# Optimization experiments

Hardware: AMD Instinct MI355X
Metric: run time of the kernel (lower is better)

## Reference

```python
import jax, jax.numpy as jnp
import numpy as np

B, H, W = 8, 640, 640
NUM_INST = 16  # upper bound on instance ids; segment reduce handles absent ids


def _bce(p, t):
    # torch BCELoss clamps log terms at -100
    lp = jnp.clip(jnp.log(p), -100.0)
    l1p = jnp.clip(jnp.log1p(-p), -100.0)
    return -(t * lp + (1.0 - t) * l1p)


def setup_inputs() -> dict:
    key = jax.random.key(0)
    k1, k2, k3, k4 = jax.random.split(key, 4)
    preds = jax.random.uniform(k1, (B, 2, H, W), dtype=jnp.float32,
                               minval=1e-4, maxval=1.0 - 1e-4)
    conf = jax.random.bernoulli(k2, 0.3, (B, H, W)).astype(jnp.float32)
    overlap = jax.random.bernoulli(k3, 0.1, (B, H, W)).astype(jnp.float32)
    inst = jax.random.randint(k4, (B, H, W), 0, NUM_INST, dtype=jnp.int32)
    inds = jnp.arange(B, dtype=jnp.int64) if jax.config.jax_enable_x64 else jnp.arange(B, dtype=jnp.int32)
    return {"preds": preds, "conf": conf, "inst": inst,
            "overlap": overlap, "inds": inds}


def reference(preds, conf, inst, overlap, inds):
    p1 = preds[:, 0]
    p2 = preds[:, 1]
    and_preds = p1 * p2
    and_loss_map = _bce(and_preds, overlap)            # [B,H,W]
    or_loss = _bce(jnp.maximum(p1, p2), conf).mean()
    and_overlap = and_preds * overlap
    op1 = jnp.maximum(p1, and_overlap)
    op2 = jnpp = jnp.maximum(p2, and_overlap)

    b, h, w = p1.shape
    # per-(sample, instance-id) segment reduce replacing the python loops.
    # MSELoss(bop*mask, mask)/sum(mask) == segment-mean of (op-1)^2 over the mask.
    seg = (jnp.arange(b, dtype=jnp.int32)[:, None, None] * NUM_INST + inst).reshape(-1)
    e1 = ((op1 - 1.0) ** 2).reshape(-1)
    e2 = ((op2 - 1.0) ** 2).reshape(-1)
    nseg = b * NUM_INST
    cnt = jax.ops.segment_sum(jnp.ones_like(e1), seg, num_segments=nseg).reshape(b, NUM_INST)
    s1 = jax.ops.segment_sum(e1, seg, num_segments=nseg).reshape(b, NUM_INST)
    s2 = jax.ops.segment_sum(e2, seg, num_segments=nseg).reshape(b, NUM_INST)
    present = cnt > 0
    safe_cnt = jnp.where(present, cnt, 1.0)
    d1 = s1 / safe_cnt
    d2 = s2 / safe_cnt
    # min(d1,d2) - max(d1,d2) + 1 == 1 - |d1 - d2|, only for present keys
    per_key = jnp.where(present, 1.0 - jnp.abs(d1 - d2), 0.0)
    nkeys = present.sum(axis=1).astype(p1.dtype)       # torch.unique count per sample
    inst_loss = (per_key.sum(axis=1) / nkeys).mean()

    pos = (conf == 1).astype(p1.dtype)
    neg = (conf == 0).astype(p1.dtype)
    and_loss = (and_loss_map * pos).sum() / pos.sum() + (and_loss_map * neg).sum() / neg.sum()

    return 0.5 * and_loss + 0.25 * or_loss + 0.25 * inst_loss
```

## Files before the change

kernel.cpp:

```cpp
#include <hip/hip_runtime.h>
#include <hip/hip_bf16.h>

#define BB 8
#define HH 640
#define WW 640
#define HWN (HH * WW)
#define NUM_INST 16
#define NBLK 128
#define NBLK_TOT (NBLK * BB)
#define THREADS 256
#define NV 36


__device__ __forceinline__ void process_pixel(
    float p1, float p2, float c, float t, int k,
    float* s12, float* cnt,
    float& accPos, float& accAll, float& accOr, float& accCnt)
{
    float andp = p1 * p2;
    bool tpos = (t != 0.0f);
    bool cpos = (c != 0.0f);
    float argA = tpos ? andp : (1.0f - andp);
    float bce_and = -fmaxf(__logf(argA), -100.0f);
    accAll += bce_and;
    accPos += cpos ? bce_and : 0.0f;
    accCnt += c;
    float mx = fmaxf(p1, p2);
    float argO = cpos ? mx : (1.0f - mx);
    accOr -= fmaxf(__logf(argO), -100.0f);
    float ao = tpos ? andp : 0.0f;
    float d1 = fmaxf(p1, ao) - 1.0f;
    float d2 = fmaxf(p2, ao) - 1.0f;
    float e12 = (d1 - d2) * (d1 + d2);
    #pragma unroll
    for (int j = 0; j < NUM_INST; ++j) {
        bool m = (k == j);
        s12[j] += m ? e12  : 0.0f;
        cnt[j] += m ? 1.0f : 0.0f;
    }
}

__global__ __launch_bounds__(THREADS) void overlap_main_kernel(
    const float* __restrict__ preds, const float* __restrict__ conf,
    const int* __restrict__ inst, const float* __restrict__ overlap,
    float* __restrict__ ws)
{
    const int b   = blockIdx.y;
    const int tid = threadIdx.x;

    const float4* p1v = (const float4*)(preds + (size_t)b * 2 * HWN);
    const float4* p2v = (const float4*)(preds + (size_t)b * 2 * HWN + HWN);
    const float4* cv  = (const float4*)(conf    + (size_t)b * HWN);
    const float4* tv  = (const float4*)(overlap + (size_t)b * HWN);
    const int4*   kv  = (const int4*)(inst      + (size_t)b * HWN);

    float vals[NV];
    #pragma unroll
    for (int v = 0; v < NV; ++v) vals[v] = 0.0f;
    float* s12 = vals;
    float* cnt = vals + 16;
    float& accPos = vals[32];
    float& accAll = vals[33];
    float& accOr  = vals[34];
    float& accCnt = vals[35];

    const int nvec   = HWN / 4;
    const int stride = gridDim.x * blockDim.x;
    for (int i = blockIdx.x * blockDim.x + tid; i < nvec; i += stride) {
        float4 A = p1v[i];
        float4 B = p2v[i];
        float4 C = cv[i];
        float4 T = tv[i];
        int4   K = kv[i];
        process_pixel(A.x, B.x, C.x, T.x, K.x, s12, cnt, accPos, accAll, accOr, accCnt);
        process_pixel(A.y, B.y, C.y, T.y, K.y, s12, cnt, accPos, accAll, accOr, accCnt);
        process_pixel(A.z, B.z, C.z, T.z, K.z, s12, cnt, accPos, accAll, accOr, accCnt);
        process_pixel(A.w, B.w, C.w, T.w, K.w, s12, cnt, accPos, accAll, accOr, accCnt);
    }

    #pragma unroll
    for (int s = 32; s > 0; s >>= 1) {
        #pragma unroll
        for (int v = 0; v < NV; ++v) vals[v] += __shfl_xor(vals[v], s, 64);
    }

    __shared__ float wsum[4][NV];
    const int wave = tid >> 6;
    const int lane = tid & 63;
    if (lane == 0) {
        #pragma unroll
        for (int v = 0; v < NV; ++v) wsum[wave][v] = vals[v];
    }
    __syncthreads();
    if (tid < NV) {
        float s = wsum[0][tid] + wsum[1][tid] + wsum[2][tid] + wsum[3][tid];
        int g = blockIdx.y * NBLK + blockIdx.x;
        ws[tid * NBLK_TOT + g] = s;
    }
}

__global__ __launch_bounds__(320) void overlap_finalize_kernel(
    const float* __restrict__ ws, float* __restrict__ out)
{
    __shared__ float seg[BB][NV];
    __shared__ float perkey[BB][NUM_INST];
    __shared__ float pres[BB][NUM_INST];
    __shared__ float binst[BB];
    const int t = threadIdx.x;

    if (t < BB * NV) {
        int b = t / NV, v = t % NV;
        const float4* p = (const float4*)(ws + v * NBLK_TOT + b * NBLK);
        float4 s4 = {0.0f, 0.0f, 0.0f, 0.0f};
        #pragma unroll 8
        for (int i = 0; i < NBLK / 4; ++i) {
            float4 q = p[i];
            s4.x += q.x; s4.y += q.y; s4.z += q.z; s4.w += q.w;
        }
        seg[b][v] = (s4.x + s4.y) + (s4.z + s4.w);
    }
    __syncthreads();

    if (t < BB * NUM_INST) {
        int b = t >> 4, k = t & 15;
        float c = seg[b][16 + k];
        bool present = c > 0.0f;
        float sc = present ? c : 1.0f;
        perkey[b][k] = present ? (1.0f - fabsf(seg[b][k]) / sc) : 0.0f;
        pres[b][k]   = present ? 1.0f : 0.0f;
    }
    __syncthreads();

    if (t < BB) {
        float s = 0.0f, nk = 0.0f;
        for (int k = 0; k < NUM_INST; ++k) { s += perkey[t][k]; nk += pres[t][k]; }
        binst[t] = s / nk;
    }
    __syncthreads();

    if (t == 0) {
        float instLoss = 0.0f, posS = 0.0f, allS = 0.0f, orS = 0.0f, posC = 0.0f;
        for (int b = 0; b < BB; ++b) {
            instLoss += binst[b];
            posS += seg[b][32];
            allS += seg[b][33];
            orS  += seg[b][34];
            posC += seg[b][35];
        }
        instLoss *= (1.0f / (float)BB);
        const float N = (float)BB * (float)HWN;
        float negS = allS - posS;
        float andLoss = posS / posC + negS / (N - posC);
        float orLoss  = orS / N;
        out[0] = 0.5f * andLoss + 0.25f * orLoss + 0.25f * instLoss;
    }
}

extern "C" void kernel_launch(void* const* d_in, const int* in_sizes, int n_in,
                              void* d_out, int out_size, void* d_ws, size_t ws_size,
                              hipStream_t stream) {
    const float* preds   = (const float*)d_in[0];
    const float* conf    = (const float*)d_in[1];
    const int*   inst    = (const int*)d_in[2];
    const float* overlap = (const float*)d_in[3];
    float* ws  = (float*)d_ws;
    float* out = (float*)d_out;

    dim3 grid(NBLK, BB);
    overlap_main_kernel<<<grid, THREADS, 0, stream>>>(preds, conf, inst, overlap, ws);
    overlap_finalize_kernel<<<1, 320, 0, stream>>>(ws, out);
}
```

Baseline: 112.5 us.

## Use exact-fit grid with all loads hoisted and ballot-based instance counts

```diff
diff --git a/kernel.cpp b/kernel.cpp
--- a/kernel.cpp
+++ b/kernel.cpp
@@ -6,25 +6,26 @@
 #define WW 640
 #define HWN (HH * WW)
 #define NUM_INST 16
-#define NBLK 128
+#define NBLK 200
 #define NBLK_TOT (NBLK * BB)
 #define THREADS 256
 #define NV 36
+#define HALF_VEC (NBLK * THREADS)
 
 
 __device__ __forceinline__ void process_pixel(
     float p1, float p2, float c, float t, int k,
-    float* s12, float* cnt,
-    float& accPos, float& accAll, float& accOr, float& accCnt)
+    float* s12, unsigned* cnt_s,
+    float& accPos, float& accAll, float& accOr, unsigned& posCnt)
 {
     float andp = p1 * p2;
     bool tpos = (t != 0.0f);
     bool cpos = (c != 0.0f);
     float argA = tpos ? andp : (1.0f - andp);
-    float bce_and = -fmaxf(__logf(argA), -100.0f);
-    accAll += bce_and;
-    accPos += cpos ? bce_and : 0.0f;
-    accCnt += c;
+    float bce = -fmaxf(__logf(argA), -100.0f);
+    accAll += bce;
+    accPos += cpos ? bce : 0.0f;
+    posCnt += (unsigned)__popcll(__ballot(cpos));
     float mx = fmaxf(p1, p2);
     float argO = cpos ? mx : (1.0f - mx);
     accOr -= fmaxf(__logf(argO), -100.0f);
@@ -35,8 +36,8 @@
     #pragma unroll
     for (int j = 0; j < NUM_INST; ++j) {
         bool m = (k == j);
-        s12[j] += m ? e12  : 0.0f;
-        cnt[j] += m ? 1.0f : 0.0f;
+        s12[j] += m ? e12 : 0.0f;
+        cnt_s[j] += (unsigned)__popcll(__ballot(m));
     }
 }
 
@@ -47,6 +48,8 @@
 {
     const int b   = blockIdx.y;
     const int tid = threadIdx.x;
+    const int i0  = blockIdx.x * THREADS + tid;
+    const int i1  = i0 + HALF_VEC;
 
     const float4* p1v = (const float4*)(preds + (size_t)b * 2 * HWN);
     const float4* p2v = (const float4*)(preds + (size_t)b * 2 * HWN + HWN);
@@ -54,34 +57,36 @@
     const float4* tv  = (const float4*)(overlap + (size_t)b * HWN);
     const int4*   kv  = (const int4*)(inst      + (size_t)b * HWN);
 
-    float vals[NV];
+    float4 A0 = p1v[i0]; float4 A1 = p1v[i1];
+    float4 B0 = p2v[i0]; float4 B1 = p2v[i1];
+    float4 C0 = cv[i0];  float4 C1 = cv[i1];
+    float4 T0 = tv[i0];  float4 T1 = tv[i1];
+    int4   K0 = kv[i0];  int4   K1 = kv[i1];
+
+    float s12[NUM_INST];
+    unsigned cnt_s[NUM_INST];
     #pragma unroll
-    for (int v = 0; v < NV; ++v) vals[v] = 0.0f;
-    float* s12 = vals;
-    float* cnt = vals + 16;
-    float& accPos = vals[32];
-    float& accAll = vals[33];
-    float& accOr  = vals[34];
-    float& accCnt = vals[35];
+    for (int j = 0; j < NUM_INST; ++j) { s12[j] = 0.0f; cnt_s[j] = 0u; }
+    float accPos = 0.0f, accAll = 0.0f, accOr = 0.0f;
+    unsigned posCnt = 0u;
 
-    const int nvec   = HWN / 4;
-    const int stride = gridDim.x * blockDim.x;
-    for (int i = blockIdx.x * blockDim.x + tid; i < nvec; i += stride) {
-        float4 A = p1v[i];
-        float4 B = p2v[i];
-        float4 C = cv[i];
-        float4 T = tv[i];
-        int4   K = kv[i];
-        process_pixel(A.x, B.x, C.x, T.x, K.x, s12, cnt, accPos, accAll, accOr, accCnt);
-        process_pixel(A.y, B.y, C.y, T.y, K.y, s12, cnt, accPos, accAll, accOr, accCnt);
-        process_pixel(A.z, B.z, C.z, T.z, K.z, s12, cnt, accPos, accAll, accOr, accCnt);
-        process_pixel(A.w, B.w, C.w, T.w, K.w, s12, cnt, accPos, accAll, accOr, accCnt);
-    }
+    process_pixel(A0.x, B0.x, C0.x, T0.x, K0.x, s12, cnt_s, accPos, accAll, accOr, posCnt);
+    process_pixel(A0.y, B0.y, C0.y, T0.y, K0.y, s12, cnt_s, accPos, accAll, accOr, posCnt);
+    process_pixel(A0.z, B0.z, C0.z, T0.z, K0.z, s12, cnt_s, accPos, accAll, accOr, posCnt);
+    process_pixel(A0.w, B0.w, C0.w, T0.w, K0.w, s12, cnt_s, accPos, accAll, accOr, posCnt);
+    process_pixel(A1.x, B1.x, C1.x, T1.x, K1.x, s12, cnt_s, accPos, accAll, accOr, posCnt);
+    process_pixel(A1.y, B1.y, C1.y, T1.y, K1.y, s12, cnt_s, accPos, accAll, accOr, posCnt);
+    process_pixel(A1.z, B1.z, C1.z, T1.z, K1.z, s12, cnt_s, accPos, accAll, accOr, posCnt);
+    process_pixel(A1.w, B1.w, C1.w, T1.w, K1.w, s12, cnt_s, accPos, accAll, accOr, posCnt);
 
+    float fv[19];
+    #pragma unroll
+    for (int j = 0; j < NUM_INST; ++j) fv[j] = s12[j];
+    fv[16] = accPos; fv[17] = accAll; fv[18] = accOr;
     #pragma unroll
     for (int s = 32; s > 0; s >>= 1) {
         #pragma unroll
-        for (int v = 0; v < NV; ++v) vals[v] += __shfl_xor(vals[v], s, 64);
+        for (int v = 0; v < 19; ++v) fv[v] += __shfl_xor(fv[v], s, 64);
     }
 
     __shared__ float wsum[4][NV];
@@ -89,7 +94,14 @@
     const int lane = tid & 63;
     if (lane == 0) {
         #pragma unroll
-        for (int v = 0; v < NV; ++v) wsum[wave][v] = vals[v];
+        for (int j = 0; j < NUM_INST; ++j) {
+            wsum[wave][j]      = fv[j];
+            wsum[wave][16 + j] = (float)cnt_s[j];
+        }
+        wsum[wave][32] = fv[16];
+        wsum[wave][33] = fv[17];
+        wsum[wave][34] = fv[18];
+        wsum[wave][35] = (float)posCnt;
     }
     __syncthreads();
     if (tid < NV) {
@@ -99,7 +111,7 @@
     }
 }
 
-__global__ __launch_bounds__(320) void overlap_finalize_kernel(
+__global__ __launch_bounds__(576) void overlap_finalize_kernel(
     const float* __restrict__ ws, float* __restrict__ out)
 {
     __shared__ float seg[BB][NV];
@@ -108,16 +120,19 @@
     __shared__ float binst[BB];
     const int t = threadIdx.x;
 
-    if (t < BB * NV) {
-        int b = t / NV, v = t % NV;
-        const float4* p = (const float4*)(ws + v * NBLK_TOT + b * NBLK);
-        float4 s4 = {0.0f, 0.0f, 0.0f, 0.0f};
-        #pragma unroll 8
-        for (int i = 0; i < NBLK / 4; ++i) {
+    {
+        int row  = t >> 1;
+        int half = t & 1;
+        int b = row / NV, v = row - b * NV;
+        const float4* p = (const float4*)(ws + v * NBLK_TOT + b * NBLK) + half * 25;
+        float s = 0.0f;
+        #pragma unroll
+        for (int i = 0; i < 25; ++i) {
             float4 q = p[i];
-            s4.x += q.x; s4.y += q.y; s4.z += q.z; s4.w += q.w;
+            s += (q.x + q.y) + (q.z + q.w);
         }
-        seg[b][v] = (s4.x + s4.y) + (s4.z + s4.w);
+        s += __shfl_xor(s, 1, 64);
+        if (half == 0) seg[b][v] = s;
     }
     __syncthreads();
 
@@ -168,5 +183,5 @@
 
     dim3 grid(NBLK, BB);
     overlap_main_kernel<<<grid, THREADS, 0, stream>>>(preds, conf, inst, overlap, ws);
-    overlap_finalize_kernel<<<1, 320, 0, stream>>>(ws, out);
+    overlap_finalize_kernel<<<1, 576, 0, stream>>>(ws, out);
 }
```

Result: slower. 117.4 us (+4.4%).

## Replace per-thread 16-way instance accumulators with shared-memory atomic histogram

Applied to the files above, without the earlier changes.

```diff
diff --git a/kernel.cpp b/kernel.cpp
--- a/kernel.cpp
+++ b/kernel.cpp
@@ -6,24 +6,29 @@
 #define WW 640
 #define HWN (HH * WW)
 #define NUM_INST 16
-#define NBLK 128
+#define NBLK 160
 #define NBLK_TOT (NBLK * BB)
 #define THREADS 256
 #define NV 36
+#define VEC_PER_BLK 640
+
+#define ROWS 128
+#define RSTRIDE 33
+#define HSIZE (ROWS * RSTRIDE)
 
 
 __device__ __forceinline__ void process_pixel(
     float p1, float p2, float c, float t, int k,
-    float* s12, float* cnt,
+    float* hrow,
     float& accPos, float& accAll, float& accOr, float& accCnt)
 {
     float andp = p1 * p2;
     bool tpos = (t != 0.0f);
     bool cpos = (c != 0.0f);
     float argA = tpos ? andp : (1.0f - andp);
-    float bce_and = -fmaxf(__logf(argA), -100.0f);
-    accAll += bce_and;
-    accPos += cpos ? bce_and : 0.0f;
+    float bce = -fmaxf(__logf(argA), -100.0f);
+    accAll += bce;
+    accPos += cpos ? bce : 0.0f;
     accCnt += c;
     float mx = fmaxf(p1, p2);
     float argO = cpos ? mx : (1.0f - mx);
@@ -32,12 +37,8 @@
     float d1 = fmaxf(p1, ao) - 1.0f;
     float d2 = fmaxf(p2, ao) - 1.0f;
     float e12 = (d1 - d2) * (d1 + d2);
-    #pragma unroll
-    for (int j = 0; j < NUM_INST; ++j) {
-        bool m = (k == j);
-        s12[j] += m ? e12  : 0.0f;
-        cnt[j] += m ? 1.0f : 0.0f;
-    }
+    atomicAdd(&hrow[k], e12);
+    atomicAdd(&hrow[k + 17], 1.0f);
 }
 
 __global__ __launch_bounds__(THREADS) void overlap_main_kernel(
@@ -45,8 +46,16 @@
     const int* __restrict__ inst, const float* __restrict__ overlap,
     float* __restrict__ ws)
 {
+    __shared__ float hist[HSIZE];
+    __shared__ float part[8][32];
+    __shared__ float wsum[4][4];
+
     const int b   = blockIdx.y;
     const int tid = threadIdx.x;
+
+    #pragma unroll
+    for (int i = tid; i < HSIZE; i += THREADS) hist[i] = 0.0f;
+    __syncthreads();
 
     const float4* p1v = (const float4*)(preds + (size_t)b * 2 * HWN);
     const float4* p2v = (const float4*)(preds + (size_t)b * 2 * HWN + HWN);
@@ -54,47 +63,75 @@
     const float4* tv  = (const float4*)(overlap + (size_t)b * HWN);
     const int4*   kv  = (const int4*)(inst      + (size_t)b * HWN);
 
-    float vals[NV];
+    float* hrow = &hist[(tid >> 1) * RSTRIDE];
+    float accPos = 0.0f, accAll = 0.0f, accOr = 0.0f, accCnt = 0.0f;
+
+    const int vbase = blockIdx.x * VEC_PER_BLK + tid;
+
     #pragma unroll
-    for (int v = 0; v < NV; ++v) vals[v] = 0.0f;
-    float* s12 = vals;
-    float* cnt = vals + 16;
-    float& accPos = vals[32];
-    float& accAll = vals[33];
-    float& accOr  = vals[34];
-    float& accCnt = vals[35];
-
-    const int nvec   = HWN / 4;
-    const int stride = gridDim.x * blockDim.x;
-    for (int i = blockIdx.x * blockDim.x + tid; i < nvec; i += stride) {
+    for (int it = 0; it < 2; ++it) {
+        const int i = vbase + it * THREADS;
         float4 A = p1v[i];
         float4 B = p2v[i];
         float4 C = cv[i];
         float4 T = tv[i];
         int4   K = kv[i];
-        process_pixel(A.x, B.x, C.x, T.x, K.x, s12, cnt, accPos, accAll, accOr, accCnt);
-        process_pixel(A.y, B.y, C.y, T.y, K.y, s12, cnt, accPos, accAll, accOr, accCnt);
-        process_pixel(A.z, B.z, C.z, T.z, K.z, s12, cnt, accPos, accAll, accOr, accCnt);
-        process_pixel(A.w, B.w, C.w, T.w, K.w, s12, cnt, accPos, accAll, accOr, accCnt);
+        process_pixel(A.x, B.x, C.x, T.x, K.x, hrow, accPos, accAll, accOr, accCnt);
+        process_pixel(A.y, B.y, C.y, T.y, K.y, hrow, accPos, accAll, accOr, accCnt);
+        process_pixel(A.z, B.z, C.z, T.z, K.z, hrow, accPos, accAll, accOr, accCnt);
+        process_pixel(A.w, B.w, C.w, T.w, K.w, hrow, accPos, accAll, accOr, accCnt);
+    }
+    if (tid < 128) {
+        const int i = vbase + 2 * THREADS;
+        float4 A = p1v[i];
+        float4 B = p2v[i];
+        float4 C = cv[i];
+        float4 T = tv[i];
+        int4   K = kv[i];
+        process_pixel(A.x, B.x, C.x, T.x, K.x, hrow, accPos, accAll, accOr, accCnt);
+        process_pixel(A.y, B.y, C.y, T.y, K.y, hrow, accPos, accAll, accOr, accCnt);
+        process_pixel(A.z, B.z, C.z, T.z, K.z, hrow, accPos, accAll, accOr, accCnt);
+        process_pixel(A.w, B.w, C.w, T.w, K.w, hrow, accPos, accAll, accOr, accCnt);
     }
 
     #pragma unroll
     for (int s = 32; s > 0; s >>= 1) {
-        #pragma unroll
-        for (int v = 0; v < NV; ++v) vals[v] += __shfl_xor(vals[v], s, 64);
-    }
-
-    __shared__ float wsum[4][NV];
+        accPos += __shfl_xor(accPos, s, 64);
+        accAll += __shfl_xor(accAll, s, 64);
+        accOr  += __shfl_xor(accOr,  s, 64);
+        accCnt += __shfl_xor(accCnt, s, 64);
+    }
     const int wave = tid >> 6;
     const int lane = tid & 63;
     if (lane == 0) {
+        wsum[wave][0] = accPos;
+        wsum[wave][1] = accAll;
+        wsum[wave][2] = accOr;
+        wsum[wave][3] = accCnt;
+    }
+    __syncthreads();
+
+    {
+        const int col = tid & 31;
+        const int grp = tid >> 5;
+        const int woff = (col < 16) ? col : (col + 1);
+        float s = 0.0f;
         #pragma unroll
-        for (int v = 0; v < NV; ++v) wsum[wave][v] = vals[v];
-    }
-    __syncthreads();
-    if (tid < NV) {
-        float s = wsum[0][tid] + wsum[1][tid] + wsum[2][tid] + wsum[3][tid];
-        int g = blockIdx.y * NBLK + blockIdx.x;
+        for (int r = 0; r < 16; ++r)
+            s += hist[(grp * 16 + r) * RSTRIDE + woff];
+        part[grp][col] = s;
+    }
+    __syncthreads();
+
+    const int g = blockIdx.y * NBLK + blockIdx.x;
+    if (tid < 32) {
+        float v = 0.0f;
+        #pragma unroll
+        for (int gr = 0; gr < 8; ++gr) v += part[gr][tid];
+        ws[tid * NBLK_TOT + g] = v;
+    } else if (tid < 36) {
+        const int v = tid - 32;
+        float s = wsum[0][v] + wsum[1][v] + wsum[2][v] + wsum[3][v];
         ws[tid * NBLK_TOT + g] = s;
     }
 }
@@ -109,7 +146,7 @@
     const int t = threadIdx.x;
 
     if (t < BB * NV) {
-        int b = t / NV, v = t % NV;
+        int b = t / NV, v = t - (t / NV) * NV;
         const float4* p = (const float4*)(ws + v * NBLK_TOT + b * NBLK);
         float4 s4 = {0.0f, 0.0f, 0.0f, 0.0f};
         #pragma unroll 8
```

Result: slower. 131.4 us (+16.8%).
